# Performance work log

Hardware: AMD Instinct MI355X
Metric: run time of the kernel (lower is better)

The kernel has to match this reference:

```python
import jax, jax.numpy as jnp
import numpy as np

B, N, C = 2, 9216, 512
HEAD, SR = 8, 4
R = 32  # lora rank
SCALING = 4.0 / 32.0  # alpha / r


def setup_inputs() -> dict:
    key = jax.random.key(0)
    ks = jax.random.split(key, 16)
    s = 0.02
    inp = {
        "x": jax.random.normal(ks[0], (B, N, C), jnp.float32),
        "w_q": jax.random.normal(ks[1], (C, C), jnp.float32) * s,
        "b_q": jnp.zeros((C,), jnp.float32),
        "w_kv": jax.random.normal(ks[2], (2 * C, C), jnp.float32) * s,
        "b_kv": jnp.zeros((2 * C,), jnp.float32),
        "w_proj": jax.random.normal(ks[3], (C, C), jnp.float32) * s,
        "b_proj": jnp.zeros((C,), jnp.float32),
        "w_sr": jax.random.normal(ks[4], (C, C, SR, SR), jnp.float32) * s,
        "b_sr": jnp.zeros((C,), jnp.float32),
        "ln_g": jnp.ones((C,), jnp.float32),
        "ln_b": jnp.zeros((C,), jnp.float32),
        "lora_A_q": jax.random.normal(ks[5], (R, C), jnp.float32) * s,
        "lora_B_q": jax.random.normal(ks[6], (C, R), jnp.float32) * s,
        "lora_A_v": jax.random.normal(ks[7], (R, C), jnp.float32) * s,
        "lora_B_v": jax.random.normal(ks[8], (C, R), jnp.float32) * s,
        "H": 96,
        "W": 96,
    }
    return inp


def reference(x, w_q, b_q, w_kv, b_kv, w_proj, b_proj, w_sr, b_sr,
              ln_g, ln_b, lora_A_q, lora_B_q, lora_A_v, lora_B_v, H, W):
    b, n, c = x.shape
    d = c // HEAD
    # q = Linear(x) + LoRA(x) * scaling
    q = x @ w_q.T + b_q + ((x @ lora_A_q.T) @ lora_B_q.T) * SCALING
    q = q.reshape(b, n, HEAD, d).transpose(0, 2, 1, 3)  # (B, h, N, d)
    # spatial reduction: Conv2d(dim, dim, sr, sr) then LayerNorm
    xi = x.transpose(0, 2, 1).reshape(b, c, H, W)
    xs = jax.lax.conv_general_dilated(
        xi, w_sr, window_strides=(SR, SR), padding='VALID',
        dimension_numbers=('NCHW', 'OIHW', 'NCHW'))
    xs = xs + b_sr[None, :, None, None]
    xs = xs.reshape(b, c, -1).transpose(0, 2, 1)  # (B, Nkv, C)
    mu = jnp.mean(xs, axis=-1, keepdims=True)
    var = jnp.var(xs, axis=-1, keepdims=True)
    xs = (xs - mu) * jax.lax.rsqrt(var + 1e-5) * ln_g + ln_b
    # k, v
    kv = (xs @ w_kv.T + b_kv).reshape(b, -1, 2, HEAD, d).transpose(2, 0, 3, 1, 4)
    k, v = kv[0], kv[1]  # (B, h, Nkv, d)
    lv = ((xs @ lora_A_v.T) @ lora_B_v.T) * SCALING  # (B, Nkv, C)
    # faithful to torch: raw memory reshape, NOT a head-transpose
    v = v + lv.reshape(b, HEAD, -1, d)
    # attention
    attn = jax.nn.softmax(jnp.einsum('bhnd,bhmd->bhnm', q, k) * (d ** -0.5), axis=-1)
    out = jnp.einsum('bhnm,bhmd->bhnd', attn, v).transpose(0, 2, 1, 3).reshape(b, n, c)
    return out @ w_proj.T + b_proj
```

## Files before the change

kernel.cpp:

```cpp
#include <hip/hip_runtime.h>

typedef __attribute__((ext_vector_type(8))) __bf16 bf16x8;
typedef __attribute__((ext_vector_type(4))) float f32x4;
typedef __attribute__((ext_vector_type(4))) unsigned int u32x4;
typedef __attribute__((ext_vector_type(2))) unsigned int u32x2;

#define MFMA16(a, b, c) __builtin_amdgcn_mfma_f32_16x16x32_bf16((a), (b), (c), 0, 0, 0)
#define QSCALE 0.18033688011112042f

__device__ __forceinline__ bool input_is_f32(const void* ln_g) {
    return ((const unsigned*)ln_g)[0] == 0x3F800000u;
}

__device__ __forceinline__ float rdf(const void* p, long i, bool f32) {
    return f32 ? ((const float*)p)[i] : (float)((const __bf16*)p)[i];
}

__device__ __forceinline__ void conv_big(const void* s, __bf16* d, long base, bool f) {
    long i = base + (long)threadIdx.x * 8;
    if (f) {
        f32x4 a = ((const f32x4*)s)[i / 4];
        f32x4 b = ((const f32x4*)s)[i / 4 + 1];
        bf16x8 o;
        #pragma unroll
        for (int j = 0; j < 4; ++j) { o[j] = (__bf16)a[j]; o[4 + j] = (__bf16)b[j]; }
        *(bf16x8*)(d + i) = o;
    } else {
        *(u32x4*)(d + i) = ((const u32x4*)s)[i / 8];
    }
}

__device__ __forceinline__ void conv_small(const void* s, __bf16* d, int n, bool f) {
    int i = threadIdx.x * 4;
    if (i < n) {
        #pragma unroll
        for (int j = 0; j < 4; ++j)
            d[i + j] = f ? (__bf16)((const float*)s)[i + j] : ((const __bf16*)s)[i + j];
    }
}

__global__ void convert_prep_kernel(const void* x, const void* w_kv, const void* w_proj,
                                    const void* b_q, const void* b_kv, const void* b_proj,
                                    const void* b_sr, const void* ln_g, const void* ln_b,
                                    const void* __restrict__ w_q,
                                    const void* __restrict__ Aq, const void* __restrict__ Bq,
                                    const void* __restrict__ Av, const void* __restrict__ Bv,
                                    const void* __restrict__ w_sr,
                                    __bf16* x_b, __bf16* w_kv_b, __bf16* w_proj_b,
                                    __bf16* b_q_b, __bf16* b_kv_b, __bf16* b_proj_b,
                                    __bf16* b_sr_b, __bf16* ln_g_b, __bf16* ln_b_b,
                                    __bf16* __restrict__ w_q_eff, __bf16* __restrict__ w_lv,
                                    __bf16* __restrict__ w_sr_t) {
    const bool f = input_is_f32(ln_g);
    int blk = blockIdx.x;
    if (blk < 4608)      conv_big(x, x_b, (long)blk * 2048, f);
    else if (blk < 4864) conv_big(w_kv, w_kv_b, (long)(blk - 4608) * 2048, f);
    else if (blk < 4992) conv_big(w_proj, w_proj_b, (long)(blk - 4864) * 2048, f);
    else if (blk == 4992) conv_small(b_q, b_q_b, 512, f);
    else if (blk == 4993) conv_small(b_kv, b_kv_b, 1024, f);
    else if (blk == 4994) conv_small(b_proj, b_proj_b, 512, f);
    else if (blk == 4995) conv_small(b_sr, b_sr_b, 512, f);
    else if (blk == 4996) conv_small(ln_g, ln_g_b, 512, f);
    else if (blk == 4997) conv_small(ln_b, ln_b_b, 512, f);
    else {
        int tid = (blk - 4998) * 256 + threadIdx.x;
        if (tid < 262144) {
            int o = tid >> 9, c = tid & 511;
            float acc = 0.f;
            #pragma unroll 8
            for (int r = 0; r < 32; ++r)
                acc += rdf(Bq, o * 32 + r, f) * rdf(Aq, r * 512 + c, f);
            w_q_eff[tid] = (__bf16)(rdf(w_q, tid, f) + 0.125f * acc);
        } else if (tid < 524288) {
            int t = tid - 262144;
            int o = t >> 9, c = t & 511;
            float acc = 0.f;
            #pragma unroll 8
            for (int r = 0; r < 32; ++r)
                acc += rdf(Bv, o * 32 + r, f) * rdf(Av, r * 512 + c, f);
            w_lv[t] = (__bf16)(0.125f * acc);
        } else if (tid < 786432) {
            int t = tid - 524288;
            int o = t >> 9, i = t & 511;
            #pragma unroll
            for (int p = 0; p < 16; ++p)
                w_sr_t[(size_t)o * 8192 + p * 512 + i] = (__bf16)rdf(w_sr, (long)t * 16 + p, f);
        }
    }
}

__global__ __launch_bounds__(256, 2) void gemm128(const __bf16* __restrict__ A,
                                                  const __bf16* __restrict__ Bt,
                                                  const __bf16* __restrict__ bias,
                                                  void* __restrict__ out, int mode) {
    __shared__ __attribute__((aligned(16))) char lds[36864];
    char* As = lds;
    char* Bs = lds + 18432;
    const int tid = threadIdx.x;
    const int m0 = blockIdx.x << 7, n0 = blockIdx.y << 7;
    const int w = tid >> 6, lane = tid & 63;
    const int wm = (w >> 1) << 6, wn = (w & 1) << 6;
    const int lr = lane & 15, lg = lane >> 4;

    f32x4 acc[4][4] = {};

    const int srow = tid >> 1;
    const int half = tid & 1;
    const __bf16* Arow = A + (size_t)(m0 + srow) * 512 + half * 32;
    const __bf16* Brow = Bt + (size_t)(n0 + srow) * 512 + half * 32;
    char* Asw = As + srow * 144 + half * 64;
    char* Bsw = Bs + srow * 144 + half * 64;

    u32x4 a0 = *(const u32x4*)(Arow);
    u32x4 a1 = *(const u32x4*)(Arow + 8);
    u32x4 a2 = *(const u32x4*)(Arow + 16);
    u32x4 a3 = *(const u32x4*)(Arow + 24);
    u32x4 b0 = *(const u32x4*)(Brow);
    u32x4 b1 = *(const u32x4*)(Brow + 8);
    u32x4 b2 = *(const u32x4*)(Brow + 16);
    u32x4 b3 = *(const u32x4*)(Brow + 24);

    for (int k0 = 0; k0 < 512; k0 += 64) {
        __syncthreads();
        *(u32x4*)(Asw) = a0;
        *(u32x4*)(Asw + 16) = a1;
        *(u32x4*)(Asw + 32) = a2;
        *(u32x4*)(Asw + 48) = a3;
        *(u32x4*)(Bsw) = b0;
        *(u32x4*)(Bsw + 16) = b1;
        *(u32x4*)(Bsw + 32) = b2;
        *(u32x4*)(Bsw + 48) = b3;
        __syncthreads();
        int kn = k0 + 64;
        if (kn < 512) {
            a0 = *(const u32x4*)(Arow + kn);
            a1 = *(const u32x4*)(Arow + kn + 8);
            a2 = *(const u32x4*)(Arow + kn + 16);
            a3 = *(const u32x4*)(Arow + kn + 24);
            b0 = *(const u32x4*)(Brow + kn);
            b1 = *(const u32x4*)(Brow + kn + 8);
            b2 = *(const u32x4*)(Brow + kn + 16);
            b3 = *(const u32x4*)(Brow + kn + 24);
        }
        bf16x8 a[4][2], b[4][2];
        #pragma unroll
        for (int i = 0; i < 4; ++i)
            #pragma unroll
            for (int ks = 0; ks < 2; ++ks)
                a[i][ks] = *(const bf16x8*)(As + (wm + i * 16 + lr) * 144 + ks * 64 + lg * 16);
        #pragma unroll
        for (int j = 0; j < 4; ++j)
            #pragma unroll
            for (int ks = 0; ks < 2; ++ks)
                b[j][ks] = *(const bf16x8*)(Bs + (wn + j * 16 + lr) * 144 + ks * 64 + lg * 16);
        #pragma unroll
        for (int i = 0; i < 4; ++i)
            #pragma unroll
            for (int j = 0; j < 4; ++j)
                #pragma unroll
                for (int ks = 0; ks < 2; ++ks)
                    acc[i][j] = MFMA16(a[i][ks], b[j][ks], acc[i][j]);
    }

    #pragma unroll
    for (int j = 0; j < 4; ++j) {
        int col = n0 + wn + j * 16 + lr;
        float bv = (float)bias[col];
        #pragma unroll
        for (int i = 0; i < 4; ++i) {
            int rb = m0 + wm + i * 16 + lg * 4;
            #pragma unroll
            for (int r = 0; r < 4; ++r) {
                float v = acc[i][j][r] + bv;
                int grow = rb + r;
                if (mode == 0) {
                    ((float*)out)[(size_t)grow * 512 + col] = v;
                } else {
                    int b_ = grow >= 9216 ? 1 : 0;
                    int nn = grow - b_ * 9216;
                    ((__bf16*)out)[(((size_t)(b_ * 8 + (col >> 6))) * 9216 + nn) * 64 +
                                   (col & 63)] = (__bf16)(v * QSCALE);
                }
            }
        }
    }
}

__global__ __launch_bounds__(256, 2) void conv_gemm(const __bf16* __restrict__ x,
                                                    const __bf16* __restrict__ Wt,
                                                    float* __restrict__ part) {
    __shared__ __attribute__((aligned(16))) char lds[36864];
    char* As = lds;
    char* Bs = lds + 18432;
    const int tid = threadIdx.x;
    const int m0 = blockIdx.x << 7, n0 = blockIdx.y << 7;
    const int kz = blockIdx.z;
    const int w = tid >> 6, lane = tid & 63;
    const int wm = (w >> 1) << 6, wn = (w & 1) << 6;
    const int lr = lane & 15, lg = lane >> 4;

    f32x4 acc[4][4] = {};

    const int srow = tid >> 1;
    const int half = tid & 1;
    int m = m0 + srow;
    int bb = m >= 576 ? 1 : 0;
    int rem = m - bb * 576;
    int oy = rem / 24;
    int ox = rem - oy * 24;
    int ky = kz >> 2, kx = kz & 3;
    const __bf16* Arow = x + ((size_t)bb * 9216 + (size_t)(oy * 384 + ky * 96 + ox * 4 + kx)) * 512
                         + half * 32;
    const __bf16* Brow = Wt + (size_t)(n0 + srow) * 8192 + kz * 512 + half * 32;
    char* Asw = As + srow * 144 + half * 64;
    char* Bsw = Bs + srow * 144 + half * 64;

    u32x4 a0 = *(const u32x4*)(Arow);
    u32x4 a1 = *(const u32x4*)(Arow + 8);
    u32x4 a2 = *(const u32x4*)(Arow + 16);
    u32x4 a3 = *(const u32x4*)(Arow + 24);
    u32x4 b0 = *(const u32x4*)(Brow);
    u32x4 b1 = *(const u32x4*)(Brow + 8);
    u32x4 b2 = *(const u32x4*)(Brow + 16);
    u32x4 b3 = *(const u32x4*)(Brow + 24);

    for (int k0 = 0; k0 < 512; k0 += 64) {
        __syncthreads();
        *(u32x4*)(Asw) = a0;
        *(u32x4*)(Asw + 16) = a1;
        *(u32x4*)(Asw + 32) = a2;
        *(u32x4*)(Asw + 48) = a3;
        *(u32x4*)(Bsw) = b0;
        *(u32x4*)(Bsw + 16) = b1;
        *(u32x4*)(Bsw + 32) = b2;
        *(u32x4*)(Bsw + 48) = b3;
        __syncthreads();
        int kn = k0 + 64;
        if (kn < 512) {
            a0 = *(const u32x4*)(Arow + kn);
            a1 = *(const u32x4*)(Arow + kn + 8);
            a2 = *(const u32x4*)(Arow + kn + 16);
            a3 = *(const u32x4*)(Arow + kn + 24);
            b0 = *(const u32x4*)(Brow + kn);
            b1 = *(const u32x4*)(Brow + kn + 8);
            b2 = *(const u32x4*)(Brow + kn + 16);
            b3 = *(const u32x4*)(Brow + kn + 24);
        }
        bf16x8 a[4][2], b[4][2];
        #pragma unroll
        for (int i = 0; i < 4; ++i)
            #pragma unroll
            for (int ks = 0; ks < 2; ++ks)
                a[i][ks] = *(const bf16x8*)(As + (wm + i * 16 + lr) * 144 + ks * 64 + lg * 16);
        #pragma unroll
        for (int j = 0; j < 4; ++j)
            #pragma unroll
            for (int ks = 0; ks < 2; ++ks)
                b[j][ks] = *(const bf16x8*)(Bs + (wn + j * 16 + lr) * 144 + ks * 64 + lg * 16);
        #pragma unroll
        for (int i = 0; i < 4; ++i)
            #pragma unroll
            for (int j = 0; j < 4; ++j)
                #pragma unroll
                for (int ks = 0; ks < 2; ++ks)
                    acc[i][j] = MFMA16(a[i][ks], b[j][ks], acc[i][j]);
    }

    float* pout = part + (size_t)kz * 589824;
    #pragma unroll
    for (int j = 0; j < 4; ++j) {
        int col = n0 + wn + j * 16 + lr;
        #pragma unroll
        for (int i = 0; i < 4; ++i) {
            int rb = m0 + wm + i * 16 + lg * 4;
            #pragma unroll
            for (int r = 0; r < 4; ++r)
                pout[(size_t)(rb + r) * 512 + col] = acc[i][j][r];
        }
    }
}

__global__ __launch_bounds__(64) void lnorm(const float* __restrict__ parts,
                                            const __bf16* __restrict__ b_sr,
                                            const __bf16* __restrict__ g,
                                            const __bf16* __restrict__ be,
                                            __bf16* __restrict__ out) {
    int row = blockIdx.x;
    int lane = threadIdx.x;
    const float* xr = parts + (size_t)row * 512;
    float v[8], s = 0.f, sq = 0.f;
    #pragma unroll
    for (int i = 0; i < 8; ++i) {
        int c = lane + i * 64;
        float t = (float)b_sr[c];
        #pragma unroll
        for (int sp = 0; sp < 16; ++sp)
            t += xr[(size_t)sp * 589824 + c];
        v[i] = t;
        s += t;
        sq += t * t;
    }
    #pragma unroll
    for (int d = 1; d < 64; d <<= 1) {
        s += __shfl_xor(s, d);
        sq += __shfl_xor(sq, d);
    }
    float mean = s * (1.0f / 512.0f);
    float var = sq * (1.0f / 512.0f) - mean * mean;
    float rstd = rsqrtf(var + 1e-5f);
    __bf16* orow = out + (size_t)row * 512;
    #pragma unroll
    for (int i = 0; i < 8; ++i) {
        int c = lane + i * 64;
        orow[c] = (__bf16)((v[i] - mean) * rstd * (float)g[c] + (float)be[c]);
    }
}

__global__ __launch_bounds__(256) void kv_gemm(const __bf16* __restrict__ xs,
                                               const __bf16* __restrict__ w_kv,
                                               const __bf16* __restrict__ w_lv,
                                               const __bf16* __restrict__ b_kv,
                                               __bf16* __restrict__ k_t,
                                               float* __restrict__ v_raw,
                                               __bf16* __restrict__ lv) {
    __shared__ __attribute__((aligned(16))) char lds[18432];
    char* As = lds;
    char* Bs = lds + 9216;
    const int tid = threadIdx.x;
    const int m0 = blockIdx.x << 6, n0 = blockIdx.y << 6;
    const int w = tid >> 6, lane = tid & 63;
    const int wm = (w >> 1) << 5, wn = (w & 1) << 5;
    const int lr = lane & 15, lg = lane >> 4;

    const int srow = tid >> 2, sc = tid & 3;
    const __bf16* arow = xs + (size_t)(m0 + srow) * 512;
    const __bf16* brow = (n0 < 1024) ? (w_kv + (size_t)(n0 + srow) * 512)
                                     : (w_lv + (size_t)(n0 - 1024 + srow) * 512);

    u32x4 pav[2], pbv[2];
    #pragma unroll
    for (int j = 0; j < 2; ++j) {
        int c = sc + j * 4;
        pav[j] = *(const u32x4*)(arow + c * 8);
        pbv[j] = *(const u32x4*)(brow + c * 8);
    }

    f32x4 acc[2][2] = {};
    for (int k0 = 0; k0 < 512; k0 += 64) {
        __syncthreads();
        #pragma unroll
        for (int j = 0; j < 2; ++j) {
            int c = sc + j * 4;
            *(u32x4*)(As + srow * 144 + c * 16) = pav[j];
            *(u32x4*)(Bs + srow * 144 + c * 16) = pbv[j];
        }
        __syncthreads();
        int kn = k0 + 64;
        if (kn < 512) {
            #pragma unroll
            for (int j = 0; j < 2; ++j) {
                int c = sc + j * 4;
                pav[j] = *(const u32x4*)(arow + kn + c * 8);
                pbv[j] = *(const u32x4*)(brow + kn + c * 8);
            }
        }
        bf16x8 a[2][2], b[2][2];
        #pragma unroll
        for (int i = 0; i < 2; ++i)
            #pragma unroll
            for (int ks = 0; ks < 2; ++ks) {
                a[i][ks] = *(const bf16x8*)(As + (wm + i * 16 + lr) * 144 + ks * 64 + lg * 16);
                b[i][ks] = *(const bf16x8*)(Bs + (wn + i * 16 + lr) * 144 + ks * 64 + lg * 16);
            }
        #pragma unroll
        for (int i = 0; i < 2; ++i)
            #pragma unroll
            for (int j = 0; j < 2; ++j)
                #pragma unroll
                for (int ks = 0; ks < 2; ++ks)
                    acc[i][j] = MFMA16(a[i][ks], b[j][ks], acc[i][j]);
    }
    #pragma unroll
    for (int j = 0; j < 2; ++j) {
        int col = n0 + wn + j * 16 + lr;
        float bv = (col < 1024) ? (float)b_kv[col] : 0.0f;
        #pragma unroll
        for (int i = 0; i < 2; ++i) {
            int rb = m0 + wm + i * 16 + lg * 4;
            #pragma unroll
            for (int r = 0; r < 4; ++r) {
                int grow = rb + r;
                float val = acc[i][j][r] + bv;
                int b_ = grow >= 576 ? 1 : 0;
                int mm = grow - b_ * 576;
                if (col < 512) {
                    int h = col >> 6, dd = col & 63;
                    k_t[(((size_t)(b_ * 8 + h)) * 576 + mm) * 64 + dd] = (__bf16)val;
                } else if (col < 1024) {
                    v_raw[((size_t)b_ * 576 + mm) * 512 + (col - 512)] = val;
                } else {
                    lv[((size_t)b_ * 576 + mm) * 512 + (col - 1024)] = (__bf16)val;
                }
            }
        }
    }
}

__global__ void v_fixup(const float* __restrict__ v_raw, const __bf16* __restrict__ lv,
                        __bf16* __restrict__ vT) {
    int tid = blockIdx.x * 256 + threadIdx.x;
    if (tid >= 589824) return;
    int mm = tid % 576;
    int rest = tid / 576;
    int dd = rest & 63;
    int bh = rest >> 6;
    int b_ = bh >> 3, h = bh & 7;
    int flat = h * 36864 + mm * 64 + dd;
    int n2 = flat >> 9, c2 = flat & 511;
    float val = v_raw[((size_t)b_ * 576 + mm) * 512 + h * 64 + dd] +
                (float)lv[((size_t)b_ * 576 + n2) * 512 + c2];
    vT[tid] = (__bf16)val;
}

__global__ __launch_bounds__(256, 2) void attn_kernel(const __bf16* __restrict__ q_t,
                                                      const __bf16* __restrict__ k_t,
                                                      const __bf16* __restrict__ vT,
                                                      __bf16* __restrict__ attnv) {
    __shared__ __attribute__((aligned(16))) char lds[18432];
    char* Ks = lds;
    char* Vs = lds + 9216;
    const int tid = threadIdx.x;
    const int w = tid >> 6, lane = tid & 63;
    const int lr = lane & 15, lg = lane >> 4;
    const int bh = blockIdx.y;
    const int qrow0 = (blockIdx.x << 8) + (w << 6);

    bf16x8 qf[4][2];
    #pragma unroll
    for (int qb = 0; qb < 4; ++qb)
        #pragma unroll
        for (int ks = 0; ks < 2; ++ks)
            qf[qb][ks] = *(const bf16x8*)(q_t + ((size_t)bh * 9216 + qrow0 + qb * 16 + lr) * 64 +
                                          ks * 32 + lg * 8);

    bf16x8 ones;
    #pragma unroll
    for (int j = 0; j < 8; ++j) ones[j] = (__bf16)1.0f;

    f32x4 oacc[4][4] = {};
    f32x4 lacc[4] = {};

    const int rr = tid >> 2, q4 = tid & 3;
    const __bf16* kg = k_t + ((size_t)bh * 576 + rr) * 64 + q4 * 16;
    char* ksw = Ks + rr * 144 + q4 * 32;
    const __bf16* vg = vT + ((size_t)bh * 64 + rr) * 576 + q4 * 16;
    char* vsw = Vs + rr * 144;
    const int offA = ((q4 & 1) << 3) | ((q4 >> 1) << 6);

    u32x4 k0v = *(const u32x4*)(kg);
    u32x4 k1v = *(const u32x4*)(kg + 8);
    u32x4 v0v = *(const u32x4*)(vg);
    u32x4 v1v = *(const u32x4*)(vg + 8);

    for (int kv0 = 0; kv0 < 576; kv0 += 64) {
        __syncthreads();
        *(u32x4*)(ksw) = k0v;
        *(u32x4*)(ksw + 16) = k1v;
        {
            u32x2 t0, t1, t2, t3;
            t0[0] = v0v[0]; t0[1] = v0v[1];
            t1[0] = v0v[2]; t1[1] = v0v[3];
            t2[0] = v1v[0]; t2[1] = v1v[1];
            t3[0] = v1v[2]; t3[1] = v1v[3];
            *(u32x2*)(vsw + offA) = t0;
            *(u32x2*)(vsw + offA + 16) = t1;
            *(u32x2*)(vsw + offA + 32) = t2;
            *(u32x2*)(vsw + offA + 48) = t3;
        }
        __syncthreads();
        int kvn = kv0 + 64;
        if (kvn < 576) {
            k0v = *(const u32x4*)(kg + (size_t)kvn * 64);
            k1v = *(const u32x4*)(kg + (size_t)kvn * 64 + 8);
            v0v = *(const u32x4*)(vg + kvn);
            v1v = *(const u32x4*)(vg + kvn + 8);
        }

        #pragma unroll
        for (int ch = 0; ch < 2; ++ch) {
            bf16x8 kf[2][2];
            #pragma unroll
            for (int kb = 0; kb < 2; ++kb)
                #pragma unroll
                for (int ks = 0; ks < 2; ++ks)
                    kf[kb][ks] = *(const bf16x8*)(Ks + ((ch * 2 + kb) * 16 + lr) * 144 +
                                                  ks * 64 + lg * 16);
            f32x4 st[2][4] = {};
            #pragma unroll
            for (int kb = 0; kb < 2; ++kb)
                #pragma unroll
                for (int qb = 0; qb < 4; ++qb)
                    #pragma unroll
                    for (int ks = 0; ks < 2; ++ks)
                        st[kb][qb] = MFMA16(kf[kb][ks], qf[qb][ks], st[kb][qb]);
            bf16x8 vf[4];
            #pragma unroll
            for (int nd = 0; nd < 4; ++nd)
                vf[nd] = *(const bf16x8*)(Vs + (nd * 16 + lr) * 144 + ch * 64 + lg * 16);
            #pragma unroll
            for (int qb = 0; qb < 4; ++qb) {
                bf16x8 pa;
                #pragma unroll
                for (int kb = 0; kb < 2; ++kb)
                    #pragma unroll
                    for (int r = 0; r < 4; ++r)
                        pa[kb * 4 + r] = (__bf16)__builtin_amdgcn_exp2f(st[kb][qb][r]);
                #pragma unroll
                for (int nd = 0; nd < 4; ++nd)
                    oacc[qb][nd] = MFMA16(pa, vf[nd], oacc[qb][nd]);
                lacc[qb] = MFMA16(pa, ones, lacc[qb]);
            }
        }
    }

    const int b_ = bh >> 3, h = bh & 7;
    #pragma unroll
    for (int qb = 0; qb < 4; ++qb) {
        f32x4 linv;
        #pragma unroll
        for (int r = 0; r < 4; ++r) linv[r] = 1.0f / lacc[qb][r];
        #pragma unroll
        for (int nd = 0; nd < 4; ++nd)
            #pragma unroll
            for (int r = 0; r < 4; ++r) {
                int row = qrow0 + qb * 16 + lg * 4 + r;
                int col = h * 64 + nd * 16 + lr;
                attnv[((size_t)b_ * 9216 + row) * 512 + col] =
                    (__bf16)(oacc[qb][nd][r] * linv[r]);
            }
    }
}

extern "C" void kernel_launch(void* const* d_in, const int* in_sizes, int n_in,
                              void* d_out, int out_size, void* d_ws, size_t ws_size,
                              hipStream_t stream) {
    const void* x      = d_in[0];
    const void* w_q    = d_in[1];
    const void* b_q    = d_in[2];
    const void* w_kv   = d_in[3];
    const void* b_kv   = d_in[4];
    const void* w_proj = d_in[5];
    const void* b_proj = d_in[6];
    const void* w_sr   = d_in[7];
    const void* b_sr   = d_in[8];
    const void* ln_g   = d_in[9];
    const void* ln_b   = d_in[10];
    const void* A_q    = d_in[11];
    const void* B_q    = d_in[12];
    const void* A_v    = d_in[13];
    const void* B_v    = d_in[14];

    char* ws = (char*)d_ws;
    __bf16* x_b      = (__bf16*)(ws);
    __bf16* attnv    = (__bf16*)(ws);
    __bf16* q_t      = (__bf16*)(ws + 18874368);
    __bf16* k_t      = (__bf16*)(ws + 37748736);
    __bf16* vT       = (__bf16*)(ws + 38928384);
    __bf16* w_q_eff  = (__bf16*)(ws + 40108032);
    __bf16* w_lv     = (__bf16*)(ws + 40632320);
    __bf16* w_sr_t   = (__bf16*)(ws + 41156608);
    __bf16* w_kv_b   = (__bf16*)(ws + 49545216);
    __bf16* w_proj_b = (__bf16*)(ws + 50593792);
    __bf16* xs_ln    = (__bf16*)(ws + 53477376);
    float*  v_raw    = (float*)(ws + 54657024);
    __bf16* lv       = (__bf16*)(ws + 57016320);
    __bf16* b_q_b    = (__bf16*)(ws + 58195968);
    __bf16* b_kv_b   = (__bf16*)(ws + 58196992);
    __bf16* b_proj_b = (__bf16*)(ws + 58199040);
    __bf16* b_sr_b   = (__bf16*)(ws + 58200064);
    __bf16* ln_g_b   = (__bf16*)(ws + 58201088);
    __bf16* ln_b_b   = (__bf16*)(ws + 58202112);
    float*  parts    = (float*)(ws + 58204160);

    convert_prep_kernel<<<8070, 256, 0, stream>>>(
        x, w_kv, w_proj, b_q, b_kv, b_proj, b_sr, ln_g, ln_b,
        w_q, A_q, B_q, A_v, B_v, w_sr,
        x_b, w_kv_b, w_proj_b, b_q_b, b_kv_b, b_proj_b, b_sr_b, ln_g_b, ln_b_b,
        w_q_eff, w_lv, w_sr_t);
    conv_gemm<<<dim3(9, 4, 16), 256, 0, stream>>>(x_b, w_sr_t, parts);
    lnorm<<<1152, 64, 0, stream>>>(parts, b_sr_b, ln_g_b, ln_b_b, xs_ln);
    gemm128<<<dim3(144, 4), 256, 0, stream>>>(x_b, w_q_eff, b_q_b, q_t, 1);
    kv_gemm<<<dim3(18, 24), 256, 0, stream>>>(xs_ln, w_kv_b, w_lv, b_kv_b, k_t, v_raw, lv);
    v_fixup<<<2304, 256, 0, stream>>>(v_raw, lv, vT);
    attn_kernel<<<dim3(36, 16), 256, 0, stream>>>(q_t, k_t, vT, attnv);
    gemm128<<<dim3(144, 4), 256, 0, stream>>>(attnv, w_proj_b, b_proj_b, d_out, 0);
}
```

Before: 273.3 us.

## Merge conv and Q GEMMs into one launch; use 64-row tiles for proj GEMM

The strided-conv split-K GEMM and the Q projection GEMM now run in a single grid of 1152 blocks, dispatched by block index, which removes one launch and lets the two independent GEMMs fill the GPU together. The output projection GEMM moves to 64x128 tiles over 1152 blocks so more blocks are resident across the CUs, at the cost of lower data reuse per tile and idle A-loading threads. Branch-dependent addressing adds a little per-block setup work.

After: 259.5 us. 1.05x faster.

```diff
diff --git a/kernel.cpp b/kernel.cpp
--- a/kernel.cpp
+++ b/kernel.cpp
@@ -89,27 +89,51 @@
     }
 }
 
-__global__ __launch_bounds__(256, 2) void gemm128(const __bf16* __restrict__ A,
-                                                  const __bf16* __restrict__ Bt,
-                                                  const __bf16* __restrict__ bias,
-                                                  void* __restrict__ out, int mode) {
+__global__ __launch_bounds__(256, 2) void qconv_gemm(const __bf16* __restrict__ x,
+                                                     const __bf16* __restrict__ Wt,
+                                                     const __bf16* __restrict__ Wq,
+                                                     const __bf16* __restrict__ bq,
+                                                     float* __restrict__ part,
+                                                     __bf16* __restrict__ q_t) {
     __shared__ __attribute__((aligned(16))) char lds[36864];
     char* As = lds;
     char* Bs = lds + 18432;
     const int tid = threadIdx.x;
-    const int m0 = blockIdx.x << 7, n0 = blockIdx.y << 7;
+    const int blk = blockIdx.x;
+    const bool isconv = blk < 576;
     const int w = tid >> 6, lane = tid & 63;
     const int wm = (w >> 1) << 6, wn = (w & 1) << 6;
     const int lr = lane & 15, lg = lane >> 4;
-
-    f32x4 acc[4][4] = {};
-
-    const int srow = tid >> 1;
-    const int half = tid & 1;
-    const __bf16* Arow = A + (size_t)(m0 + srow) * 512 + half * 32;
-    const __bf16* Brow = Bt + (size_t)(n0 + srow) * 512 + half * 32;
+    const int srow = tid >> 1, half = tid & 1;
+
+    int m0, n0, kzv = 0;
+    const __bf16 *Arow, *Brow;
+    if (isconv) {
+        int mb = blk % 9;
+        int rest = blk / 9;
+        int nb = rest & 3;
+        kzv = rest >> 2;
+        m0 = mb << 7; n0 = nb << 7;
+        int m = m0 + srow;
+        int bb = m >= 576 ? 1 : 0;
+        int rem = m - bb * 576;
+        int oy = rem / 24;
+        int ox = rem - oy * 24;
+        int ky = kzv >> 2, kx = kzv & 3;
+        Arow = x + ((size_t)bb * 9216 + (size_t)(oy * 384 + ky * 96 + ox * 4 + kx)) * 512
+               + half * 32;
+        Brow = Wt + (size_t)(n0 + srow) * 8192 + kzv * 512 + half * 32;
+    } else {
+        int b2 = blk - 576;
+        int mb = b2 % 144, nb = b2 / 144;
+        m0 = mb << 7; n0 = nb << 7;
+        Arow = x + (size_t)(m0 + srow) * 512 + half * 32;
+        Brow = Wq + (size_t)(n0 + srow) * 512 + half * 32;
+    }
     char* Asw = As + srow * 144 + half * 64;
     char* Bsw = Bs + srow * 144 + half * 64;
+
+    f32x4 acc[4][4] = {};
 
     u32x4 a0 = *(const u32x4*)(Arow);
     u32x4 a1 = *(const u32x4*)(Arow + 8);
@@ -162,63 +186,69 @@
                     acc[i][j] = MFMA16(a[i][ks], b[j][ks], acc[i][j]);
     }
 
-    #pragma unroll
-    for (int j = 0; j < 4; ++j) {
-        int col = n0 + wn + j * 16 + lr;
-        float bv = (float)bias[col];
-        #pragma unroll
-        for (int i = 0; i < 4; ++i) {
-            int rb = m0 + wm + i * 16 + lg * 4;
-            #pragma unroll
-            for (int r = 0; r < 4; ++r) {
-                float v = acc[i][j][r] + bv;
-                int grow = rb + r;
-                if (mode == 0) {
-                    ((float*)out)[(size_t)grow * 512 + col] = v;
-                } else {
+    if (isconv) {
+        float* pout = part + (size_t)kzv * 589824;
+        #pragma unroll
+        for (int j = 0; j < 4; ++j) {
+            int col = n0 + wn + j * 16 + lr;
+            #pragma unroll
+            for (int i = 0; i < 4; ++i) {
+                int rb = m0 + wm + i * 16 + lg * 4;
+                #pragma unroll
+                for (int r = 0; r < 4; ++r)
+                    pout[(size_t)(rb + r) * 512 + col] = acc[i][j][r];
+            }
+        }
+    } else {
+        #pragma unroll
+        for (int j = 0; j < 4; ++j) {
+            int col = n0 + wn + j * 16 + lr;
+            float bv = (float)bq[col];
+            #pragma unroll
+            for (int i = 0; i < 4; ++i) {
+                int rb = m0 + wm + i * 16 + lg * 4;
+                #pragma unroll
+                for (int r = 0; r < 4; ++r) {
+                    int grow = rb + r;
                     int b_ = grow >= 9216 ? 1 : 0;
                     int nn = grow - b_ * 9216;
-                    ((__bf16*)out)[(((size_t)(b_ * 8 + (col >> 6))) * 9216 + nn) * 64 +
-                                   (col & 63)] = (__bf16)(v * QSCALE);
+                    q_t[(((size_t)(b_ * 8 + (col >> 6))) * 9216 + nn) * 64 + (col & 63)] =
+                        (__bf16)((acc[i][j][r] + bv) * QSCALE);
                 }
             }
         }
     }
 }
 
-__global__ __launch_bounds__(256, 2) void conv_gemm(const __bf16* __restrict__ x,
-                                                    const __bf16* __restrict__ Wt,
-                                                    float* __restrict__ part) {
-    __shared__ __attribute__((aligned(16))) char lds[36864];
+__global__ __launch_bounds__(256, 2) void proj_gemm(const __bf16* __restrict__ A,
+                                                    const __bf16* __restrict__ Bt,
+                                                    const __bf16* __restrict__ bias,
+                                                    float* __restrict__ out) {
+    __shared__ __attribute__((aligned(16))) char lds[27648];
     char* As = lds;
-    char* Bs = lds + 18432;
+    char* Bs = lds + 9216;
     const int tid = threadIdx.x;
-    const int m0 = blockIdx.x << 7, n0 = blockIdx.y << 7;
-    const int kz = blockIdx.z;
+    const int m0 = blockIdx.x << 6, n0 = blockIdx.y << 7;
     const int w = tid >> 6, lane = tid & 63;
-    const int wm = (w >> 1) << 6, wn = (w & 1) << 6;
+    const int wm = (w >> 1) << 5, wn = (w & 1) << 6;
     const int lr = lane & 15, lg = lane >> 4;
 
-    f32x4 acc[4][4] = {};
-
-    const int srow = tid >> 1;
-    const int half = tid & 1;
-    int m = m0 + srow;
-    int bb = m >= 576 ? 1 : 0;
-    int rem = m - bb * 576;
-    int oy = rem / 24;
-    int ox = rem - oy * 24;
-    int ky = kz >> 2, kx = kz & 3;
-    const __bf16* Arow = x + ((size_t)bb * 9216 + (size_t)(oy * 384 + ky * 96 + ox * 4 + kx)) * 512
-                         + half * 32;
-    const __bf16* Brow = Wt + (size_t)(n0 + srow) * 8192 + kz * 512 + half * 32;
-    char* Asw = As + srow * 144 + half * 64;
+    f32x4 acc[2][4] = {};
+
+    const int srow = tid >> 1, half = tid & 1;
+    const bool doA = tid < 128;
+    const __bf16* Arow = A + (size_t)(m0 + (srow & 63)) * 512 + half * 32;
+    const __bf16* Brow = Bt + (size_t)(n0 + srow) * 512 + half * 32;
+    char* Asw = As + (srow & 63) * 144 + half * 64;
     char* Bsw = Bs + srow * 144 + half * 64;
 
-    u32x4 a0 = *(const u32x4*)(Arow);
-    u32x4 a1 = *(const u32x4*)(Arow + 8);
-    u32x4 a2 = *(const u32x4*)(Arow + 16);
-    u32x4 a3 = *(const u32x4*)(Arow + 24);
+    u32x4 a0{}, a1{}, a2{}, a3{};
+    if (doA) {
+        a0 = *(const u32x4*)(Arow);
+        a1 = *(const u32x4*)(Arow + 8);
+        a2 = *(const u32x4*)(Arow + 16);
+        a3 = *(const u32x4*)(Arow + 24);
+    }
     u32x4 b0 = *(const u32x4*)(Brow);
     u32x4 b1 = *(const u32x4*)(Brow + 8);
     u32x4 b2 = *(const u32x4*)(Brow + 16);
@@ -226,10 +256,12 @@
 
     for (int k0 = 0; k0 < 512; k0 += 64) {
         __syncthreads();
-        *(u32x4*)(Asw) = a0;
-        *(u32x4*)(Asw + 16) = a1;
-        *(u32x4*)(Asw + 32) = a2;
-        *(u32x4*)(Asw + 48) = a3;
+        if (doA) {
+            *(u32x4*)(Asw) = a0;
+            *(u32x4*)(Asw + 16) = a1;
+            *(u32x4*)(Asw + 32) = a2;
+            *(u32x4*)(Asw + 48) = a3;
+        }
         *(u32x4*)(Bsw) = b0;
         *(u32x4*)(Bsw + 16) = b1;
         *(u32x4*)(Bsw + 32) = b2;
@@ -237,18 +269,20 @@
         __syncthreads();
         int kn = k0 + 64;
         if (kn < 512) {
-            a0 = *(const u32x4*)(Arow + kn);
-            a1 = *(const u32x4*)(Arow + kn + 8);
-            a2 = *(const u32x4*)(Arow + kn + 16);
-            a3 = *(const u32x4*)(Arow + kn + 24);
+            if (doA) {
+                a0 = *(const u32x4*)(Arow + kn);
+                a1 = *(const u32x4*)(Arow + kn + 8);
+                a2 = *(const u32x4*)(Arow + kn + 16);
+                a3 = *(const u32x4*)(Arow + kn + 24);
+            }
             b0 = *(const u32x4*)(Brow + kn);
             b1 = *(const u32x4*)(Brow + kn + 8);
             b2 = *(const u32x4*)(Brow + kn + 16);
             b3 = *(const u32x4*)(Brow + kn + 24);
         }
-        bf16x8 a[4][2], b[4][2];
-        #pragma unroll
-        for (int i = 0; i < 4; ++i)
+        bf16x8 a[2][2], b[4][2];
+        #pragma unroll
+        for (int i = 0; i < 2; ++i)
             #pragma unroll
             for (int ks = 0; ks < 2; ++ks)
                 a[i][ks] = *(const bf16x8*)(As + (wm + i * 16 + lr) * 144 + ks * 64 + lg * 16);
@@ -258,7 +292,7 @@
             for (int ks = 0; ks < 2; ++ks)
                 b[j][ks] = *(const bf16x8*)(Bs + (wn + j * 16 + lr) * 144 + ks * 64 + lg * 16);
         #pragma unroll
-        for (int i = 0; i < 4; ++i)
+        for (int i = 0; i < 2; ++i)
             #pragma unroll
             for (int j = 0; j < 4; ++j)
                 #pragma unroll
@@ -266,16 +300,16 @@
                     acc[i][j] = MFMA16(a[i][ks], b[j][ks], acc[i][j]);
     }
 
-    float* pout = part + (size_t)kz * 589824;
     #pragma unroll
     for (int j = 0; j < 4; ++j) {
         int col = n0 + wn + j * 16 + lr;
-        #pragma unroll
-        for (int i = 0; i < 4; ++i) {
+        float bv = (float)bias[col];
+        #pragma unroll
+        for (int i = 0; i < 2; ++i) {
             int rb = m0 + wm + i * 16 + lg * 4;
             #pragma unroll
             for (int r = 0; r < 4; ++r)
-                pout[(size_t)(rb + r) * 512 + col] = acc[i][j][r];
+                out[(size_t)(rb + r) * 512 + col] = acc[i][j][r] + bv;
         }
     }
 }
@@ -587,11 +621,10 @@
         w_q, A_q, B_q, A_v, B_v, w_sr,
         x_b, w_kv_b, w_proj_b, b_q_b, b_kv_b, b_proj_b, b_sr_b, ln_g_b, ln_b_b,
         w_q_eff, w_lv, w_sr_t);
-    conv_gemm<<<dim3(9, 4, 16), 256, 0, stream>>>(x_b, w_sr_t, parts);
+    qconv_gemm<<<1152, 256, 0, stream>>>(x_b, w_sr_t, w_q_eff, b_q_b, parts, q_t);
     lnorm<<<1152, 64, 0, stream>>>(parts, b_sr_b, ln_g_b, ln_b_b, xs_ln);
-    gemm128<<<dim3(144, 4), 256, 0, stream>>>(x_b, w_q_eff, b_q_b, q_t, 1);
     kv_gemm<<<dim3(18, 24), 256, 0, stream>>>(xs_ln, w_kv_b, w_lv, b_kv_b, k_t, v_raw, lv);
     v_fixup<<<2304, 256, 0, stream>>>(v_raw, lv, vT);
     attn_kernel<<<dim3(36, 16), 256, 0, stream>>>(q_t, k_t, vT, attnv);
-    gemm128<<<dim3(144, 4), 256, 0, stream>>>(attnv, w_proj_b, b_proj_b, d_out, 0);
-}
+    proj_gemm<<<dim3(288, 4), 256, 0, stream>>>(attnv, w_proj_b, b_proj_b, (float*)d_out);
+}
```
